# Performance work log

Hardware: AMD Instinct MI355X
Metric: run time of the kernel (lower is better)

## Reference

```python
import jax, jax.numpy as jnp
import numpy as np

# --- batched state-vector quantum circuit sim: AngleEmbedding(RY) + BasicEntanglerLayers(RX + ring CNOT) ---

def _ry(state, theta, wire, n):
    # per-sample RY(theta) on `wire`; state: (B,) + (2,)*n complex
    ax = wire + 1
    c = jnp.cos(0.5 * theta).reshape((-1,) + (1,) * (n - 1)).astype(state.dtype)
    s = jnp.sin(0.5 * theta).reshape((-1,) + (1,) * (n - 1)).astype(state.dtype)
    s0 = jnp.take(state, 0, axis=ax)
    s1 = jnp.take(state, 1, axis=ax)
    return jnp.stack([c * s0 - s * s1, s * s0 + c * s1], axis=ax)

def _rx(state, theta, wire, n):
    # scalar RX(theta) on `wire` (shared weight across batch)
    ax = wire + 1
    c = jnp.cos(0.5 * theta).astype(state.dtype)
    s = (-1j * jnp.sin(0.5 * theta)).astype(state.dtype)
    s0 = jnp.take(state, 0, axis=ax)
    s1 = jnp.take(state, 1, axis=ax)
    return jnp.stack([c * s0 + s * s1, s * s0 + c * s1], axis=ax)

def _cnot(state, ctrl, tgt):
    ax_c = ctrl + 1
    s0 = jnp.take(state, 0, axis=ax_c)
    s1 = jnp.take(state, 1, axis=ax_c)
    ax_t = tgt + 1 if tgt < ctrl else tgt  # target axis index after removing ctrl axis
    s1 = jnp.flip(s1, axis=ax_t)
    return jnp.stack([s0, s1], axis=ax_c)

def _circuit(x_qin, qweights):
    # x_qin: (Bn, n) angles; qweights: (L, n)
    Bn, n = x_qin.shape
    state = jnp.zeros((Bn,) + (2,) * n, jnp.complex64)
    state = state.at[(slice(None),) + (0,) * n].set(1.0)
    for w in range(n):  # AngleEmbedding, rotation='Y'
        state = _ry(state, x_qin[:, w], w, n)
    for l in range(qweights.shape[0]):  # BasicEntanglerLayers
        for w in range(n):
            state = _rx(state, qweights[l, w], w, n)
        for w in range(n):
            state = _cnot(state, w, (w + 1) % n)
    probs = jnp.real(state * jnp.conj(state))
    outs = []
    for w in range(n):  # <Z_w> = P(bit_w=0) - P(bit_w=1)
        axes = tuple(a for a in range(1, n + 1) if a != w + 1)
        p = probs.sum(axis=axes)  # (Bn, 2)
        outs.append(p[:, 0] - p[:, 1])
    return jnp.stack(outs, axis=-1).astype(jnp.float32)


def setup_inputs() -> dict:
    key = jax.random.key(0)
    ks = jax.random.split(key, 9)
    B, N, H, NQ, L = 16, 1024, 256, 8, 2
    x = jax.random.normal(ks[0], (B, N, H), jnp.float32)
    norm_adj = jax.random.uniform(ks[1], (N, N), jnp.float32) / N
    Wg = jax.random.normal(ks[2], (H, H), jnp.float32) * 0.02
    bg = jax.random.normal(ks[3], (H,), jnp.float32) * 0.02
    Wpre = jax.random.normal(ks[4], (NQ, H), jnp.float32) * 0.05
    bpre = jax.random.normal(ks[5], (NQ,), jnp.float32) * 0.02
    qweights = jax.random.uniform(ks[6], (L, NQ), jnp.float32) * (2.0 * np.pi)
    Wpost = jax.random.normal(ks[7], (H, NQ), jnp.float32) * 0.1
    bpost = jax.random.normal(ks[8], (H,), jnp.float32) * 0.02
    return {"x": x, "norm_adj": norm_adj, "Wg": Wg, "bg": bg, "Wpre": Wpre,
            "bpre": bpre, "qweights": qweights, "Wpost": Wpost, "bpost": bpost}


def reference(x, norm_adj, Wg, bg, Wpre, bpre, qweights, Wpost, bpost):
    # GCN aggregation + GELU(Linear)  (dropout is identity in eval mode)
    x_agg = jnp.einsum('ij,bjh->bih', norm_adj, x)
    x_agg = jax.nn.gelu(x_agg @ Wg.T + bg, approximate=False)
    B, N, H = x_agg.shape
    x_flat = x_agg.reshape(B * N, H).astype(jnp.float32)
    x_qin = jnp.tanh(x_flat @ Wpre.T + bpre) * np.pi
    q_out = _circuit(x_qin, qweights)          # (B*N, n_qubits)
    out = (q_out @ Wpost.T + bpost).reshape(B, N, H)
    return out
```

## Files before the change

kernel.cpp:

```cpp
#include <hip/hip_runtime.h>
#include <math.h>

typedef __attribute__((ext_vector_type(8))) short bf16x8;
typedef _Float16 f16x8 __attribute__((ext_vector_type(8)));
typedef __attribute__((ext_vector_type(4))) float f32x4;

#define PI_F 3.14159265358979323846f

__device__ __forceinline__ unsigned short f2bf(float f) {
  unsigned int u = __float_as_uint(f);
  u += 0x7FFFu + ((u >> 16) & 1u);
  return (unsigned short)(u >> 16);
}

__device__ __forceinline__ float bf2f(unsigned short u) {
  return __uint_as_float(((unsigned int)u) << 16);
}

__device__ __forceinline__ void async_ld16(const unsigned short* g, unsigned short* l) {
  __builtin_amdgcn_global_load_lds(
      (const __attribute__((address_space(1))) void*)g,
      (__attribute__((address_space(3))) void*)l,
      16, 0, 0);
}

__device__ __forceinline__ float fast_erf(float x) {
  float a = fabsf(x);
  float t = 1.0f / fmaf(0.3275911f, a, 1.0f);
  float p = t * fmaf(t, fmaf(t, fmaf(t, fmaf(t, 1.061405429f, -1.453152027f),
                                     1.421413741f), -0.284496736f), 0.254829592f);
  float e = __expf(-a * a);
  float r = 1.0f - p * e;
  return copysignf(r, x);
}

__device__ __forceinline__ float fast_tanh(float a) {
  float e = __expf(2.0f * a);
  return 1.0f - 2.0f / (e + 1.0f);
}

template<int ML, int MR>
__device__ __forceinline__ void apply_rx(float re[4], float im[4], float c, float s) {
  float pr[4], pi[4];
  #pragma unroll
  for (int r = 0; r < 4; r++) {
    float vr = re[r ^ MR], vi = im[r ^ MR];
    if (ML) { vr = __shfl_xor(vr, ML, 64); vi = __shfl_xor(vi, ML, 64); }
    pr[r] = vr; pi[r] = vi;
  }
  #pragma unroll
  for (int r = 0; r < 4; r++) {
    re[r] = fmaf(c, re[r],  s * pi[r]);
    im[r] = fmaf(c, im[r], -s * pr[r]);
  }
}

__global__ __launch_bounds__(256)
void prep_kernel(const float* __restrict__ adj, unsigned short* __restrict__ adj_bf,
                 const float* __restrict__ Wg, unsigned short* __restrict__ Wg_bf,
                 const float* __restrict__ qw, unsigned short* __restrict__ Uri,
                 const float* __restrict__ Wpost, _Float16* __restrict__ Gt,
                 const float* __restrict__ x, unsigned short* __restrict__ xT) {
  __shared__ float smem[1056];
  int bid = blockIdx.x, t = threadIdx.x;
  if (bid < 1024) {
    int i = bid * 256 + t;
    float4 v = ((const float4*)adj)[i];
    ushort4 o; o.x = f2bf(v.x); o.y = f2bf(v.y); o.z = f2bf(v.z); o.w = f2bf(v.w);
    ((ushort4*)adj_bf)[i] = o;
  } else if (bid < 1088) {
    int i = (bid - 1024) * 256 + t;
    float4 v = ((const float4*)Wg)[i];
    ushort4 o; o.x = f2bf(v.x); o.y = f2bf(v.y); o.z = f2bf(v.z); o.w = f2bf(v.w);
    ((ushort4*)Wg_bf)[i] = o;
  } else if (bid < 1152) {
    if (t < 16) { smem[t] = cosf(0.5f * qw[t]); smem[16 + t] = sinf(0.5f * qw[t]); }
    __syncthreads();
    int wv = t >> 6, L = t & 63;
    int k = (bid - 1088) * 4 + wv;
    float re[4], im[4];
    #pragma unroll
    for (int r = 0; r < 4; r++) { re[r] = (r * 64 + L == k) ? 1.f : 0.f; im[r] = 0.f; }
    apply_rx<1, 0>(re, im, smem[0], smem[16]);
    apply_rx<2, 0>(re, im, smem[1], smem[17]);
    apply_rx<4, 0>(re, im, smem[2], smem[18]);
    apply_rx<8, 0>(re, im, smem[3], smem[19]);
    apply_rx<16, 0>(re, im, smem[4], smem[20]);
    apply_rx<32, 0>(re, im, smem[5], smem[21]);
    apply_rx<0, 1>(re, im, smem[6], smem[22]);
    apply_rx<0, 2>(re, im, smem[7], smem[23]);
    apply_rx<3, 0>(re, im, smem[8], smem[24]);
    apply_rx<6, 0>(re, im, smem[9], smem[25]);
    apply_rx<12, 0>(re, im, smem[10], smem[26]);
    apply_rx<24, 0>(re, im, smem[11], smem[27]);
    apply_rx<48, 0>(re, im, smem[12], smem[28]);
    apply_rx<32, 1>(re, im, smem[13], smem[29]);
    apply_rx<0, 3>(re, im, smem[14], smem[30]);
    apply_rx<3, 2>(re, im, smem[15], smem[31]);
    const int M[8] = {0xAB, 0xFD, 0xFA, 0xF5, 0xEA, 0xD5, 0xAA, 0x55};
    #pragma unroll
    for (int r = 0; r < 4; r++) {
      int n = 0;
      #pragma unroll
      for (int w = 0; w < 8; w++) {
        int bit = (__popc(L & (M[w] & 63)) ^ __popc((r << 6) & M[w])) & 1;
        n |= bit << w;
      }
      int row_re = ((n >> 4) << 5) + (n & 15);
      Uri[(size_t)row_re * 256 + k] = f2bf(re[r]);
      Uri[(size_t)(row_re + 16) * 256 + k] = f2bf(im[r]);
    }
  } else if (bid < 1168) {
    int tid = (bid - 1152) * 256 + t;
    int h = tid >> 4;
    int n0 = (tid & 15) << 4;
    float wv8[8];
    #pragma unroll
    for (int w = 0; w < 8; w++) wv8[w] = Wpost[h * 8 + w];
    #pragma unroll
    for (int j = 0; j < 16; j++) {
      int n = n0 + j;
      float sum = 0.f;
      #pragma unroll
      for (int w = 0; w < 8; w++) sum += ((n >> w) & 1) ? -wv8[w] : wv8[w];
      Gt[h * 256 + n] = (_Float16)sum;
    }
  } else {
    int tb = bid - 1168;
    int jt = tb & 31, ht = (tb >> 5) & 7, bb = tb >> 8;
    const float* xb = x + (size_t)bb * 1024 * 256;
    int row = t >> 3, cg = t & 7;
    {
      float4 v = *(const float4*)&xb[(size_t)(jt * 32 + row) * 256 + ht * 32 + cg * 4];
      smem[row * 33 + cg * 4 + 0] = v.x;
      smem[row * 33 + cg * 4 + 1] = v.y;
      smem[row * 33 + cg * 4 + 2] = v.z;
      smem[row * 33 + cg * 4 + 3] = v.w;
    }
    __syncthreads();
    unsigned short* xTb = xT + (size_t)bb * 256 * 1024;
    int h = ht * 32 + row;
    ushort4 o;
    o.x = f2bf(smem[(cg * 4 + 0) * 33 + row]);
    o.y = f2bf(smem[(cg * 4 + 1) * 33 + row]);
    o.z = f2bf(smem[(cg * 4 + 2) * 33 + row]);
    o.w = f2bf(smem[(cg * 4 + 3) * 33 + row]);
    *(ushort4*)&xTb[(size_t)h * 1024 + jt * 32 + cg * 4] = o;
  }
}

__global__ __launch_bounds__(256)
void gemm1_kernel(const unsigned short* __restrict__ A,
                  const unsigned short* __restrict__ Bt,
                  unsigned short* __restrict__ C,
                  int K, int tilesN, int ldC) {
  __shared__ unsigned short As[2 * 2 * 64 * 32];
  __shared__ unsigned short Bs[2 * 2 * 128 * 32];
  int bid = blockIdx.x;
  int swz = (bid & 7) * 64 + (bid >> 3);
  int in_ = swz >> 4;
  int im  = swz & 15;
  const unsigned short* Ab  = A  + (long long)im * 64 * K;
  const unsigned short* Btb = Bt + (long long)in_ * 128 * K;

  int t = threadIdx.x;
  int wv = t >> 6, lane = t & 63;
  int wm = wv >> 1, wn = wv & 1;
  int l15 = lane & 15, quad = lane >> 4;

  int ra  = t >> 2,        ca  = (t & 3) ^ ((ra >> 1) & 3);
  int rb1 = (256 + t) >> 2, cb1 = ((256 + t) & 3) ^ ((rb1 >> 1) & 3);
  long long goA  = (long long)ra * K + ca * 8;
  long long goB0 = (long long)ra * K + ca * 8;
  long long goB1 = (long long)rb1 * K + cb1 * 8;

  f32x4 acc[2][4] = {};

  #pragma unroll
  for (int kb = 0; kb < 2; kb++) {
    async_ld16(Ab + goA + kb * 32, &As[kb * 2048 + t * 8]);
    async_ld16(Btb + goB0 + kb * 32, &Bs[kb * 4096 + t * 8]);
    async_ld16(Btb + goB1 + kb * 32, &Bs[kb * 4096 + (256 + t) * 8]);
  }
  __syncthreads();

  int nk = K >> 6;
  for (int ki = 0; ki < nk; ki++) {
    int buf = ki & 1;
    if (ki + 1 < nk) {
      int nb = buf ^ 1;
      long long kk = (long long)(ki + 1) << 6;
      #pragma unroll
      for (int kb = 0; kb < 2; kb++) {
        async_ld16(Ab + goA + kk + kb * 32, &As[nb * 4096 + kb * 2048 + t * 8]);
        async_ld16(Btb + goB0 + kk + kb * 32, &Bs[nb * 8192 + kb * 4096 + t * 8]);
        async_ld16(Btb + goB1 + kk + kb * 32, &Bs[nb * 8192 + kb * 4096 + (256 + t) * 8]);
      }
    }
    #pragma unroll
    for (int kb = 0; kb < 2; kb++) {
      bf16x8 af[2], bfr[4];
      #pragma unroll
      for (int mt = 0; mt < 2; mt++) {
        int row = wm * 32 + mt * 16 + l15;
        af[mt] = *(const bf16x8*)&As[buf * 4096 + kb * 2048 + row * 32 +
                                     ((quad ^ ((row >> 1) & 3)) * 8)];
      }
      #pragma unroll
      for (int nt = 0; nt < 4; nt++) {
        int row = wn * 64 + nt * 16 + l15;
        bfr[nt] = *(const bf16x8*)&Bs[buf * 8192 + kb * 4096 + row * 32 +
                                      ((quad ^ ((row >> 1) & 3)) * 8)];
      }
      #pragma unroll
      for (int mt = 0; mt < 2; mt++)
        #pragma unroll
        for (int nt = 0; nt < 4; nt++)
          acc[mt][nt] = __builtin_amdgcn_mfma_f32_16x16x32_bf16(af[mt], bfr[nt], acc[mt][nt], 0, 0, 0);
    }
    __syncthreads();
  }

  int n0 = in_ * 128;
  #pragma unroll
  for (int mt = 0; mt < 2; mt++) {
    #pragma unroll
    for (int nt = 0; nt < 4; nt++) {
      int colg = n0 + wn * 64 + nt * 16 + l15;
      #pragma unroll
      for (int r = 0; r < 4; r++) {
        int rowg = im * 64 + wm * 32 + mt * 16 + quad * 4 + r;
        C[(size_t)rowg * ldC + colg] = f2bf(acc[mt][nt][r]);
      }
    }
  }
}

__global__ __launch_bounds__(1024, 4)
void qfused_kernel(const unsigned short* __restrict__ xagg,
                   const unsigned short* __restrict__ Wg,
                   const float* __restrict__ bg,
                   const float* __restrict__ Wpre, const float* __restrict__ bpre,
                   const unsigned short* __restrict__ Uri,
                   const _Float16* __restrict__ Gt,
                   const float* __restrict__ bpost,
                   float* __restrict__ out) {
  __shared__ __align__(16) char smemraw[102400];
  unsigned short* As  = (unsigned short*)smemraw;
  unsigned short* gs  = (unsigned short*)(smemraw + 32768);
  _Float16*       Ts  = (_Float16*)(smemraw + 32768);
  unsigned short* P0s = (unsigned short*)(smemraw + 65536);
  float*          prt = (float*)(smemraw + 65536);
  float*          csw = (float*)(smemraw + 98304);

  int t = threadIdx.x;
  int wv = t >> 6, lane = t & 63;
  int l15 = lane & 15, quad = lane >> 4;

  const unsigned short* Ab = xagg + (size_t)blockIdx.x * 64 * 256;

  #pragma unroll
  for (int q = 0; q < 2; q++) {
    int sidx = q * 1024 + t;
    int kb = sidx >> 8;
    int r  = (sidx >> 2) & 63;
    int c  = (sidx & 3) ^ ((r >> 1) & 3);
    async_ld16(Ab + (size_t)r * 256 + kb * 32 + c * 8, &As[sidx * 8]);
  }
  __syncthreads();

  f32x4 acc[4] = {};
  {
    const unsigned short* Wp = Wg + (size_t)(wv * 16 + l15) * 256 + quad * 8;
    bf16x8 wf[2];
    wf[0] = *(const bf16x8*)(Wp);
    wf[1] = *(const bf16x8*)(Wp + 32);
    #pragma unroll
    for (int k8 = 0; k8 < 8; k8++) {
      int cur = k8 & 1;
      #pragma unroll
      for (int mt = 0; mt < 4; mt++) {
        int row = mt * 16 + l15;
        bf16x8 af = *(const bf16x8*)&As[k8 * 2048 + row * 32 + ((quad ^ ((row >> 1) & 3)) * 8)];
        acc[mt] = __builtin_amdgcn_mfma_f32_16x16x32_bf16(af, wf[cur], acc[mt], 0, 0, 0);
      }
      if (k8 < 6) wf[cur] = *(const bf16x8*)(Wp + (k8 + 2) * 32);
    }
  }
  {
    int col = wv * 16 + l15;
    float bgl = bg[col];
    int kbc = col >> 5, chunk = (col >> 3) & 3, e = col & 7;
    #pragma unroll
    for (int mt = 0; mt < 4; mt++) {
      #pragma unroll
      for (int r = 0; r < 4; r++) {
        int row = mt * 16 + quad * 4 + r;
        float v = acc[mt][r] + bgl;
        v = 0.5f * v * (1.0f + fast_erf(v * 0.7071067811865475f));
        *(unsigned short*)((char*)gs + kbc * 4096 + row * 64 +
                           ((chunk ^ ((row >> 1) & 3)) << 4) + e * 2) = f2bf(v);
      }
    }
  }
  __syncthreads();

  {
    int k8 = wv >> 1, mh = wv & 1;
    const float* wrow = Wpre + (size_t)(l15 & 7) * 256 + k8 * 32 + quad * 8;
    float4 wa = *(const float4*)wrow;
    float4 wb = *(const float4*)(wrow + 4);
    float v8[8] = {wa.x, wa.y, wa.z, wa.w, wb.x, wb.y, wb.z, wb.w};
    bf16x8 whi, wlo;
    #pragma unroll
    for (int j = 0; j < 8; j++) {
      unsigned short h = f2bf(v8[j]);
      whi[j] = (short)h;
      wlo[j] = (short)f2bf(v8[j] - bf2f(h));
    }
    f32x4 aacc[2] = {};
    #pragma unroll
    for (int mt = 0; mt < 2; mt++) {
      int row = mh * 32 + mt * 16 + l15;
      bf16x8 ga = *(const bf16x8*)((char*)gs + k8 * 4096 + row * 64 +
                                   ((quad ^ ((row >> 1) & 3)) << 4));
      aacc[mt] = __builtin_amdgcn_mfma_f32_16x16x32_bf16(ga, whi, aacc[mt], 0, 0, 0);
      aacc[mt] = __builtin_amdgcn_mfma_f32_16x16x32_bf16(ga, wlo, aacc[mt], 0, 0, 0);
    }
    if (l15 < 8) {
      #pragma unroll
      for (int mt = 0; mt < 2; mt++)
        #pragma unroll
        for (int r = 0; r < 4; r++)
          prt[k8 * 512 + (mh * 32 + mt * 16 + quad * 4 + r) * 8 + l15] = aacc[mt][r];
    }
  }
  __syncthreads();

  if (t < 512) {
    float s = 0.f;
    #pragma unroll
    for (int k = 0; k < 8; k++) s += prt[k * 512 + t];
    float th = (0.5f * PI_F) * fast_tanh(s + bpre[t & 7]);
    int row = t >> 3, w = t & 7;
    csw[row * 16 + w] = __cosf(th);
    csw[row * 16 + 8 + w] = __sinf(th);
  }
  __syncthreads();

  #pragma unroll
  for (int rr = 0; rr < 4; rr++) {
    int row = wv * 4 + rr;
    float4 c0 = *(const float4*)&csw[row * 16];
    float4 c1 = *(const float4*)&csw[row * 16 + 4];
    float4 s0 = *(const float4*)&csw[row * 16 + 8];
    float4 s1 = *(const float4*)&csw[row * 16 + 12];
    float cw[8] = {c0.x, c0.y, c0.z, c0.w, c1.x, c1.y, c1.z, c1.w};
    float sw[8] = {s0.x, s0.y, s0.z, s0.w, s1.x, s1.y, s1.z, s1.w};
    float pl = 1.f;
    #pragma unroll
    for (int b = 0; b < 6; b++) pl *= ((lane >> b) & 1) ? sw[b + 2] : cw[b + 2];
    ushort4 o;
    o.x = f2bf(pl * cw[0] * cw[1]);
    o.y = f2bf(pl * sw[0] * cw[1]);
    o.z = f2bf(pl * cw[0] * sw[1]);
    o.w = f2bf(pl * sw[0] * sw[1]);
    int jj = lane & 7;
    int cswz = (jj >> 1) ^ ((row >> 1) & 3);
    *(ushort4*)((char*)P0s + (lane >> 3) * 4096 + row * 64 + cswz * 16 + (jj & 1) * 8) = o;
  }
  __syncthreads();

  f32x4 acc1[4][2] = {};
  {
    const unsigned short* Up = Uri + (size_t)(wv * 32 + l15) * 256 + quad * 8;
    bf16x8 ua[2][2];
    #pragma unroll
    for (int sl = 0; sl < 2; sl++)
      #pragma unroll
      for (int nt = 0; nt < 2; nt++)
        ua[sl][nt] = *(const bf16x8*)(Up + sl * 32 + nt * 4096);
    #pragma unroll
    for (int k8 = 0; k8 < 8; k8++) {
      int cur = k8 & 1;
      #pragma unroll
      for (int mt = 0; mt < 4; mt++) {
        int row = mt * 16 + l15;
        bf16x8 pa = *(const bf16x8*)((char*)P0s + k8 * 4096 + row * 64 +
                                     ((quad ^ ((row >> 1) & 3)) << 4));
        acc1[mt][0] = __builtin_amdgcn_mfma_f32_16x16x32_bf16(pa, ua[cur][0], acc1[mt][0], 0, 0, 0);
        acc1[mt][1] = __builtin_amdgcn_mfma_f32_16x16x32_bf16(pa, ua[cur][1], acc1[mt][1], 0, 0, 0);
      }
      if (k8 < 6) {
        #pragma unroll
        for (int nt = 0; nt < 2; nt++)
          ua[cur][nt] = *(const bf16x8*)(Up + (k8 + 2) * 32 + nt * 4096);
      }
    }
  }

  {
    int colT = wv * 16 + l15;
    int kbc = colT >> 5, chunk = (colT >> 3) & 3, e = colT & 7;
    #pragma unroll
    for (int mt = 0; mt < 4; mt++) {
      #pragma unroll
      for (int r = 0; r < 4; r++) {
        int row = mt * 16 + quad * 4 + r;
        float tre = acc1[mt][0][r], tim = acc1[mt][1][r];
        *(_Float16*)((char*)Ts + kbc * 4096 + row * 64 +
                     ((chunk ^ ((row >> 1) & 3)) << 4) + e * 2)
            = (_Float16)(tre * tre + tim * tim);
      }
    }
  }
  __syncthreads();

  f32x4 acc2[4] = {};
  {
    const _Float16* Gp = Gt + (size_t)(wv * 16 + l15) * 256 + quad * 8;
    f16x8 gf[2];
    gf[0] = *(const f16x8*)(Gp);
    gf[1] = *(const f16x8*)(Gp + 32);
    #pragma unroll
    for (int k8 = 0; k8 < 8; k8++) {
      int cur = k8 & 1;
      #pragma unroll
      for (int mt = 0; mt < 4; mt++) {
        int row = mt * 16 + l15;
        f16x8 tf = *(const f16x8*)((char*)Ts + k8 * 4096 + row * 64 +
                                   ((quad ^ ((row >> 1) & 3)) << 4));
        acc2[mt] = __builtin_amdgcn_mfma_f32_16x16x32_f16(tf, gf[cur], acc2[mt], 0, 0, 0);
      }
      if (k8 < 6) gf[cur] = *(const f16x8*)(Gp + (k8 + 2) * 32);
    }
  }

  {
    int col = wv * 16 + l15;
    float bp = bpost[col];
    #pragma unroll
    for (int mt = 0; mt < 4; mt++) {
      #pragma unroll
      for (int r = 0; r < 4; r++) {
        int row = mt * 16 + quad * 4 + r;
        int s = blockIdx.x * 64 + row;
        int orow = (s & 15) * 1024 + (s >> 4);
        out[(size_t)orow * 256 + col] = acc2[mt][r] + bp;
      }
    }
  }
}

extern "C" void kernel_launch(void* const* d_in, const int* in_sizes, int n_in,
                              void* d_out, int out_size, void* d_ws, size_t ws_size,
                              hipStream_t stream) {
  const float* x     = (const float*)d_in[0];
  const float* adj   = (const float*)d_in[1];
  const float* Wg    = (const float*)d_in[2];
  const float* bg    = (const float*)d_in[3];
  const float* Wpre  = (const float*)d_in[4];
  const float* bpre  = (const float*)d_in[5];
  const float* qw    = (const float*)d_in[6];
  const float* Wpost = (const float*)d_in[7];
  const float* bpost = (const float*)d_in[8];
  float* out = (float*)d_out;

  char* ws = (char*)d_ws;
  unsigned short* adj_bf  = (unsigned short*)(ws + 0);
  unsigned short* Wg_bf   = (unsigned short*)(ws + 2097152);
  unsigned short* xT_bf   = (unsigned short*)(ws + 2228224);
  unsigned short* xagg_bf = (unsigned short*)(ws + 10616832);
  unsigned short* Uri     = (unsigned short*)(ws + 19005440);
  _Float16*       Gt      = (_Float16*)(ws + 19267584);

  prep_kernel<<<5264, 256, 0, stream>>>(adj, adj_bf, Wg, Wg_bf, qw, Uri,
                                        Wpost, Gt, x, xT_bf);

  gemm1_kernel<<<512, 256, 0, stream>>>(adj_bf, xT_bf, xagg_bf, 1024, 32, 4096);

  qfused_kernel<<<256, 1024, 0, stream>>>(xagg_bf, Wg_bf, bg, Wpre, bpre, Uri, Gt, bpost, out);
}
```

Before: 129.2 us.

## Enlarge GEMM1 tile to 128x128 and hoist weight loads above barriers

The adjacency GEMM now computes 128x128 output tiles instead of 64x128, with each wave owning a 64x64 sub-tile. This halves the grid to 256 blocks and increases reuse of each loaded B tile, cutting global and LDS traffic per MFMA. The cost is more accumulator registers and fewer blocks, which lowers occupancy and leaves fewer blocks than the GPU has compute units. In the fused quantum kernel, weight-fragment loads for the three MFMA stages are issued before the preceding barriers so their global latency overlaps the sync. The first stage now preloads all eight fragments, which raises register pressure.

```diff
diff --git a/kernel.cpp b/kernel.cpp
--- a/kernel.cpp
+++ b/kernel.cpp
@@ -154,13 +154,13 @@
                   const unsigned short* __restrict__ Bt,
                   unsigned short* __restrict__ C,
                   int K, int tilesN, int ldC) {
-  __shared__ unsigned short As[2 * 2 * 64 * 32];
+  __shared__ unsigned short As[2 * 2 * 128 * 32];
   __shared__ unsigned short Bs[2 * 2 * 128 * 32];
   int bid = blockIdx.x;
-  int swz = (bid & 7) * 64 + (bid >> 3);
-  int in_ = swz >> 4;
-  int im  = swz & 15;
-  const unsigned short* Ab  = A  + (long long)im * 64 * K;
+  int swz = (bid & 7) * 32 + (bid >> 3);
+  int in_ = swz >> 3;
+  int im  = swz & 7;
+  const unsigned short* Ab  = A  + (long long)im * 128 * K;
   const unsigned short* Btb = Bt + (long long)in_ * 128 * K;
 
   int t = threadIdx.x;
@@ -168,19 +168,19 @@
   int wm = wv >> 1, wn = wv & 1;
   int l15 = lane & 15, quad = lane >> 4;
 
-  int ra  = t >> 2,        ca  = (t & 3) ^ ((ra >> 1) & 3);
-  int rb1 = (256 + t) >> 2, cb1 = ((256 + t) & 3) ^ ((rb1 >> 1) & 3);
-  long long goA  = (long long)ra * K + ca * 8;
-  long long goB0 = (long long)ra * K + ca * 8;
-  long long goB1 = (long long)rb1 * K + cb1 * 8;
-
-  f32x4 acc[2][4] = {};
+  int r0 = t >> 2,         c0 = (t & 3) ^ ((r0 >> 1) & 3);
+  int r1 = (256 + t) >> 2, c1 = (t & 3) ^ ((r1 >> 1) & 3);
+  long long go0 = (long long)r0 * K + c0 * 8;
+  long long go1 = (long long)r1 * K + c1 * 8;
+
+  f32x4 acc[4][4] = {};
 
   #pragma unroll
   for (int kb = 0; kb < 2; kb++) {
-    async_ld16(Ab + goA + kb * 32, &As[kb * 2048 + t * 8]);
-    async_ld16(Btb + goB0 + kb * 32, &Bs[kb * 4096 + t * 8]);
-    async_ld16(Btb + goB1 + kb * 32, &Bs[kb * 4096 + (256 + t) * 8]);
+    async_ld16(Ab + go0 + kb * 32, &As[kb * 4096 + t * 8]);
+    async_ld16(Ab + go1 + kb * 32, &As[kb * 4096 + (256 + t) * 8]);
+    async_ld16(Btb + go0 + kb * 32, &Bs[kb * 4096 + t * 8]);
+    async_ld16(Btb + go1 + kb * 32, &Bs[kb * 4096 + (256 + t) * 8]);
   }
   __syncthreads();
 
@@ -192,18 +192,19 @@
       long long kk = (long long)(ki + 1) << 6;
       #pragma unroll
       for (int kb = 0; kb < 2; kb++) {
-        async_ld16(Ab + goA + kk + kb * 32, &As[nb * 4096 + kb * 2048 + t * 8]);
-        async_ld16(Btb + goB0 + kk + kb * 32, &Bs[nb * 8192 + kb * 4096 + t * 8]);
-        async_ld16(Btb + goB1 + kk + kb * 32, &Bs[nb * 8192 + kb * 4096 + (256 + t) * 8]);
+        async_ld16(Ab + go0 + kk + kb * 32, &As[nb * 8192 + kb * 4096 + t * 8]);
+        async_ld16(Ab + go1 + kk + kb * 32, &As[nb * 8192 + kb * 4096 + (256 + t) * 8]);
+        async_ld16(Btb + go0 + kk + kb * 32, &Bs[nb * 8192 + kb * 4096 + t * 8]);
+        async_ld16(Btb + go1 + kk + kb * 32, &Bs[nb * 8192 + kb * 4096 + (256 + t) * 8]);
       }
     }
     #pragma unroll
     for (int kb = 0; kb < 2; kb++) {
-      bf16x8 af[2], bfr[4];
-      #pragma unroll
-      for (int mt = 0; mt < 2; mt++) {
-        int row = wm * 32 + mt * 16 + l15;
-        af[mt] = *(const bf16x8*)&As[buf * 4096 + kb * 2048 + row * 32 +
+      bf16x8 af[4], bfr[4];
+      #pragma unroll
+      for (int mt = 0; mt < 4; mt++) {
+        int row = wm * 64 + mt * 16 + l15;
+        af[mt] = *(const bf16x8*)&As[buf * 8192 + kb * 4096 + row * 32 +
                                      ((quad ^ ((row >> 1) & 3)) * 8)];
       }
       #pragma unroll
@@ -213,7 +214,7 @@
                                       ((quad ^ ((row >> 1) & 3)) * 8)];
       }
       #pragma unroll
-      for (int mt = 0; mt < 2; mt++)
+      for (int mt = 0; mt < 4; mt++)
         #pragma unroll
         for (int nt = 0; nt < 4; nt++)
           acc[mt][nt] = __builtin_amdgcn_mfma_f32_16x16x32_bf16(af[mt], bfr[nt], acc[mt][nt], 0, 0, 0);
@@ -223,13 +224,13 @@
 
   int n0 = in_ * 128;
   #pragma unroll
-  for (int mt = 0; mt < 2; mt++) {
+  for (int mt = 0; mt < 4; mt++) {
     #pragma unroll
     for (int nt = 0; nt < 4; nt++) {
       int colg = n0 + wn * 64 + nt * 16 + l15;
       #pragma unroll
       for (int r = 0; r < 4; r++) {
-        int rowg = im * 64 + wm * 32 + mt * 16 + quad * 4 + r;
+        int rowg = im * 128 + wm * 64 + mt * 16 + quad * 4 + r;
         C[(size_t)rowg * ldC + colg] = f2bf(acc[mt][nt][r]);
       }
     }
@@ -267,24 +268,20 @@
     int c  = (sidx & 3) ^ ((r >> 1) & 3);
     async_ld16(Ab + (size_t)r * 256 + kb * 32 + c * 8, &As[sidx * 8]);
   }
+  const unsigned short* Wp = Wg + (size_t)(wv * 16 + l15) * 256 + quad * 8;
+  bf16x8 wf[8];
+  #pragma unroll
+  for (int k8 = 0; k8 < 8; k8++) wf[k8] = *(const bf16x8*)(Wp + k8 * 32);
   __syncthreads();
 
   f32x4 acc[4] = {};
-  {
-    const unsigned short* Wp = Wg + (size_t)(wv * 16 + l15) * 256 + quad * 8;
-    bf16x8 wf[2];
-    wf[0] = *(const bf16x8*)(Wp);
-    wf[1] = *(const bf16x8*)(Wp + 32);
-    #pragma unroll
-    for (int k8 = 0; k8 < 8; k8++) {
-      int cur = k8 & 1;
-      #pragma unroll
-      for (int mt = 0; mt < 4; mt++) {
-        int row = mt * 16 + l15;
-        bf16x8 af = *(const bf16x8*)&As[k8 * 2048 + row * 32 + ((quad ^ ((row >> 1) & 3)) * 8)];
-        acc[mt] = __builtin_amdgcn_mfma_f32_16x16x32_bf16(af, wf[cur], acc[mt], 0, 0, 0);
-      }
-      if (k8 < 6) wf[cur] = *(const bf16x8*)(Wp + (k8 + 2) * 32);
+  #pragma unroll
+  for (int k8 = 0; k8 < 8; k8++) {
+    #pragma unroll
+    for (int mt = 0; mt < 4; mt++) {
+      int row = mt * 16 + l15;
+      bf16x8 af = *(const bf16x8*)&As[k8 * 2048 + row * 32 + ((quad ^ ((row >> 1) & 3)) * 8)];
+      acc[mt] = __builtin_amdgcn_mfma_f32_16x16x32_bf16(af, wf[k8], acc[mt], 0, 0, 0);
     }
   }
   {
@@ -369,17 +366,17 @@
     int cswz = (jj >> 1) ^ ((row >> 1) & 3);
     *(ushort4*)((char*)P0s + (lane >> 3) * 4096 + row * 64 + cswz * 16 + (jj & 1) * 8) = o;
   }
+  const unsigned short* Up = Uri + (size_t)(wv * 32 + l15) * 256 + quad * 8;
+  bf16x8 ua[2][2];
+  #pragma unroll
+  for (int sl = 0; sl < 2; sl++)
+    #pragma unroll
+    for (int nt = 0; nt < 2; nt++)
+      ua[sl][nt] = *(const bf16x8*)(Up + sl * 32 + nt * 4096);
   __syncthreads();
 
   f32x4 acc1[4][2] = {};
   {
-    const unsigned short* Up = Uri + (size_t)(wv * 32 + l15) * 256 + quad * 8;
-    bf16x8 ua[2][2];
-    #pragma unroll
-    for (int sl = 0; sl < 2; sl++)
-      #pragma unroll
-      for (int nt = 0; nt < 2; nt++)
-        ua[sl][nt] = *(const bf16x8*)(Up + sl * 32 + nt * 4096);
     #pragma unroll
     for (int k8 = 0; k8 < 8; k8++) {
       int cur = k8 & 1;
@@ -414,14 +411,14 @@
       }
     }
   }
+  const _Float16* Gp = Gt + (size_t)(wv * 16 + l15) * 256 + quad * 8;
+  f16x8 gf[2];
+  gf[0] = *(const f16x8*)(Gp);
+  gf[1] = *(const f16x8*)(Gp + 32);
   __syncthreads();
 
   f32x4 acc2[4] = {};
   {
-    const _Float16* Gp = Gt + (size_t)(wv * 16 + l15) * 256 + quad * 8;
-    f16x8 gf[2];
-    gf[0] = *(const f16x8*)(Gp);
-    gf[1] = *(const f16x8*)(Gp + 32);
     #pragma unroll
     for (int k8 = 0; k8 < 8; k8++) {
       int cur = k8 & 1;
@@ -477,7 +474,7 @@
   prep_kernel<<<5264, 256, 0, stream>>>(adj, adj_bf, Wg, Wg_bf, qw, Uri,
                                         Wpost, Gt, x, xT_bf);
 
-  gemm1_kernel<<<512, 256, 0, stream>>>(adj_bf, xT_bf, xagg_bf, 1024, 32, 4096);
+  gemm1_kernel<<<256, 256, 0, stream>>>(adj_bf, xT_bf, xagg_bf, 1024, 32, 4096);
 
   qfused_kernel<<<256, 1024, 0, stream>>>(xagg_bf, Wg_bf, bg, Wpre, bpre, Uri, Gt, bpost, out);
 }
```

Result: slower. 133.4 us (+3.2%).
